# Kernel tuning notes

Hardware: AMD Instinct MI355X
Metric: run time of the kernel (lower is better)

The kernel has to match this reference:

```python
import jax, jax.numpy as jnp
import numpy as np

N_NODES = 50000
N_EDGES = 800000
D = 128
N_LAYERS = 4


def _sage_conv(x, edge_index, Wl, bl, Wr):
    # PyG SAGEConv (mean aggr): out = lin_l(mean_{j in N(i)} x_j) + lin_r(x_i)
    src, dst = edge_index[0], edge_index[1]
    msgs = x[src]                                            # [E, D] gather
    summed = jax.ops.segment_sum(msgs, dst, num_segments=N_NODES)   # [N, D]
    cnt = jax.ops.segment_sum(jnp.ones((msgs.shape[0],), x.dtype), dst,
                              num_segments=N_NODES)
    mean = summed / jnp.maximum(cnt, 1.0)[:, None]           # [N, D]
    return mean @ Wl.T + bl + x @ Wr.T


def setup_inputs() -> dict:
    key = jax.random.key(0)
    ks = jax.random.split(key, 2 + 3 * N_LAYERS)
    x = jax.random.normal(ks[0], (N_NODES, D), dtype=jnp.float32)
    edge_index = jax.random.randint(ks[1], (2, N_EDGES), 0, N_NODES, dtype=jnp.int64)
    inp = {"x": x, "edge_index": edge_index}
    s = 1.0 / np.sqrt(D)
    for i in range(N_LAYERS):
        inp[f"Wl{i}"] = jax.random.uniform(ks[2 + 3 * i], (D, D), jnp.float32, -s, s)
        inp[f"bl{i}"] = jax.random.uniform(ks[3 + 3 * i], (D,), jnp.float32, -s, s)
        inp[f"Wr{i}"] = jax.random.uniform(ks[4 + 3 * i], (D, D), jnp.float32, -s, s)
    return inp


def reference(x, edge_index, Wl0, bl0, Wr0, Wl1, bl1, Wr1, Wl2, bl2, Wr2, Wl3, bl3, Wr3):
    # ReLU only after the first conv, per the original forward.
    h = jax.nn.relu(_sage_conv(x, edge_index, Wl0, bl0, Wr0))
    h = _sage_conv(h, edge_index, Wl1, bl1, Wr1)
    h = _sage_conv(h, edge_index, Wl2, bl2, Wr2)
    h = _sage_conv(h, edge_index, Wl3, bl3, Wr3)
    return h
```

## Files before the change

### kernel.cpp

```cpp
#include <hip/hip_runtime.h>
#include <stdint.h>

#define NN 50000
#define NE 800000
#define CAST_B 6250
#define CVTW_B 512
#define EPB 8192
#define HIST_B 98
#define NBK 196

typedef short short8 __attribute__((ext_vector_type(8)));
typedef float f32x4 __attribute__((ext_vector_type(4)));
typedef unsigned int uint;
typedef unsigned short ushort;

__device__ __forceinline__ uint rne_bf16(float f) {
    uint x = __float_as_uint(f);
    return (x + 0x7FFFu + ((x >> 16) & 1u)) >> 16;
}
__device__ __forceinline__ float bf_lo(uint d) { return __uint_as_float(d << 16); }
__device__ __forceinline__ float bf_hi(uint d) { return __uint_as_float(d & 0xFFFF0000u); }

__device__ __forceinline__ int ei_is64(const int* __restrict__ ei) {
    return (ei[1] | ei[3] | ei[5] | ei[7]) == 0;
}

struct Ptrs8 { const float* p[8]; };

__global__ __launch_bounds__(256) void k_prep(
    const float* __restrict__ x, ushort* __restrict__ xbf, Ptrs8 ps,
    ushort* __restrict__ wbf, const int* __restrict__ ei,
    uint* __restrict__ ebuf, int* __restrict__ hcnt) {
    __shared__ int hs[NBK];
    int b = blockIdx.x;
    if (b < CAST_B) {
        int i = b * 256 + threadIdx.x;
        float4 v = ((const float4*)x)[i];
        uint2 o;
        o.x = rne_bf16(v.x) | (rne_bf16(v.y) << 16);
        o.y = rne_bf16(v.z) | (rne_bf16(v.w) << 16);
        ((uint2*)xbf)[i] = o;
    } else if (b < CAST_B + CVTW_B) {
        int idx = (b - CAST_B) * 256 + threadIdx.x;
        int m = idx >> 14;
        int o14 = idx & 16383;
        int k0i = (o14 >> 12) & 3;
        int t = (o14 >> 9) & 7;
        int lane6 = (o14 >> 3) & 63;
        int e = o14 & 7;
        int r = t * 16 + (lane6 & 15);
        int c = k0i * 32 + (lane6 >> 4) * 8 + e;
        wbf[idx] = (ushort)rne_bf16(ps.p[m][r * 128 + c]);
    } else {
        int hb = b - CAST_B - CVTW_B;
        int t = threadIdx.x;
        for (int i = t; i < NBK; i += 256) hs[i] = 0;
        __syncthreads();
        int base = hb * EPB;
        int is64 = ei_is64(ei);
        for (int i = 0; i < EPB; i += 256) {
            int e = base + i + t;
            if (e < NE) {
                int sv = is64 ? ei[2 * e] : ei[e];
                int dv = is64 ? ei[2 * NE + 2 * e] : ei[NE + e];
                ebuf[e] = ((uint)dv << 16) | (uint)sv;
                atomicAdd(&hs[dv >> 8], 1);
            }
        }
        __syncthreads();
        for (int i = t; i < NBK; i += 256) hcnt[hb * NBK + i] = hs[i];
    }
}

__global__ __launch_bounds__(256) void k_scan1(const int* __restrict__ hcnt,
                                               int* __restrict__ hoff,
                                               int* __restrict__ bb,
                                               int* __restrict__ row_ptr) {
    __shared__ int s[256];
    int t = threadIdx.x;
    int tot = 0;
    if (t < NBK)
        for (int b = 0; b < HIST_B; b++) tot += hcnt[b * NBK + t];
    s[t] = tot;
    __syncthreads();
    for (int off = 1; off < 256; off <<= 1) {
        int v = s[t];
        int a = (t >= off) ? s[t - off] : 0;
        __syncthreads();
        s[t] = v + a;
        __syncthreads();
    }
    if (t < NBK) {
        int base = (t == 0) ? 0 : s[t - 1];
        bb[t] = base;
        int run = base;
        for (int b = 0; b < HIST_B; b++) {
            hoff[b * NBK + t] = run;
            run += hcnt[b * NBK + t];
        }
    }
    if (t == 0) { bb[NBK] = NE; row_ptr[NN] = NE; }
}

__global__ __launch_bounds__(256) void k_scatter1(const uint* __restrict__ ebuf,
                                                  const int* __restrict__ hoff,
                                                  uint* __restrict__ ebuf2) {
    __shared__ int pos[NBK];
    int hb = blockIdx.x, t = threadIdx.x;
    for (int i = t; i < NBK; i += 256) pos[i] = hoff[hb * NBK + i];
    __syncthreads();
    int base = hb * EPB;
    for (int i = 0; i < EPB; i += 256) {
        int e = base + i + t;
        if (e < NE) {
            uint pk = ebuf[e];
            int idx = atomicAdd(&pos[pk >> 24], 1);
            ebuf2[idx] = pk;
        }
    }
}

__global__ __launch_bounds__(1024) void k_sort2(const uint* __restrict__ ebuf2,
                                                const int* __restrict__ bb,
                                                int* __restrict__ row_ptr,
                                                ushort* __restrict__ col) {
    __shared__ int hist[256];
    __shared__ int pos[256];
    int k = blockIdx.x, t = threadIdx.x;
    int beg = bb[k], end = bb[k + 1];
    if (t < 256) hist[t] = 0;
    __syncthreads();
    for (int j = beg + t; j < end; j += 1024)
        atomicAdd(&hist[(ebuf2[j] >> 16) & 255], 1);
    __syncthreads();
    for (int off = 1; off < 256; off <<= 1) {
        int v = 0;
        if (t < 256) { v = hist[t]; if (t >= off) v += hist[t - off]; }
        __syncthreads();
        if (t < 256) hist[t] = v;
        __syncthreads();
    }
    if (t < 256) {
        int ex = (t == 0) ? 0 : hist[t - 1];
        pos[t] = beg + ex;
        int node = k * 256 + t;
        if (node < NN) row_ptr[node] = beg + ex;
    }
    __syncthreads();
    for (int j = beg + t; j < end; j += 1024) {
        uint pk = ebuf2[j];
        int idx = atomicAdd(&pos[(pk >> 16) & 255], 1);
        col[idx] = (ushort)(pk & 0xFFFFu);
    }
}

__global__ __launch_bounds__(256) void k_agg3(const ushort* __restrict__ h,
                                              const int* __restrict__ row_ptr,
                                              const ushort* __restrict__ col,
                                              ushort* __restrict__ mean) {
    int node = blockIdx.x * 4 + (threadIdx.x >> 6);
    if (node >= NN) return;
    int lane = threadIdx.x & 63;
    int beg = row_ptr[node], end = row_ptr[node + 1];
    const uint* hp = (const uint*)h;
    float a0 = 0.f, a1 = 0.f;
    for (int b = beg; b < end; b += 64) {
        int n = min(64, end - b);
        int c = (int)col[b + min(lane, n - 1)];
        for (int j0 = 0; j0 < n; j0 += 8) {
#pragma unroll
            for (int j = 0; j < 8; j++) {
                int jj = j0 + j;
                int s = __shfl(c, min(jj, n - 1));
                uint v = hp[s * 64 + lane];
                float m = (jj < n) ? 1.f : 0.f;
                a0 = fmaf(m, bf_lo(v), a0);
                a1 = fmaf(m, bf_hi(v), a1);
            }
        }
    }
    float r = 1.0f / (float)max(end - beg, 1);
    ((uint*)mean)[node * 64 + lane] = rne_bf16(a0 * r) | (rne_bf16(a1 * r) << 16);
}

__global__ __launch_bounds__(256) void k_gemm_mfma(
    const ushort* __restrict__ Am, const ushort* __restrict__ Ah,
    const ushort* __restrict__ Wlb, const ushort* __restrict__ Wrb,
    const float* __restrict__ bias, float* __restrict__ outf,
    ushort* __restrict__ outb, int relu) {
    const int lane = threadIdx.x & 63;
    const int wave = threadIdx.x >> 6;
    const int l15 = lane & 15;
    const int quad = lane >> 4;
    const int m0 = blockIdx.x * 128 + wave * 32;

    f32x4 acc[2][8];
#pragma unroll
    for (int s = 0; s < 2; s++)
#pragma unroll
        for (int t = 0; t < 8; t++) acc[s][t] = (f32x4){0.f, 0.f, 0.f, 0.f};

    int ar0 = min(m0 + l15, NN - 1);
    int ar1 = min(m0 + 16 + l15, NN - 1);
    const ushort* A0m = Am + (size_t)ar0 * 128 + quad * 8;
    const ushort* A1m = Am + (size_t)ar1 * 128 + quad * 8;
    const ushort* A0h = Ah + (size_t)ar0 * 128 + quad * 8;
    const ushort* A1h = Ah + (size_t)ar1 * 128 + quad * 8;

#pragma unroll
    for (int half = 0; half < 2; half++) {
        const ushort* W = half ? Wrb : Wlb;
        const ushort* A0 = half ? A0h : A0m;
        const ushort* A1 = half ? A1h : A1m;
#pragma unroll
        for (int k0 = 0; k0 < 128; k0 += 32) {
            short8 a0 = *(const short8*)(A0 + k0);
            short8 a1 = *(const short8*)(A1 + k0);
            const ushort* Wk = W + ((k0 >> 5) * 8) * 512 + lane * 8;
#pragma unroll
            for (int t = 0; t < 8; t++) {
                short8 b = *(const short8*)(Wk + t * 512);
                acc[0][t] = __builtin_amdgcn_mfma_f32_16x16x32_bf16(a0, b, acc[0][t], 0, 0, 0);
                acc[1][t] = __builtin_amdgcn_mfma_f32_16x16x32_bf16(a1, b, acc[1][t], 0, 0, 0);
            }
        }
    }

    float bb[8];
#pragma unroll
    for (int t = 0; t < 8; t++) bb[t] = bias[t * 16 + l15];

#pragma unroll
    for (int s = 0; s < 2; s++) {
#pragma unroll
        for (int r = 0; r < 4; r++) {
            int row = m0 + s * 16 + quad * 4 + r;
            if (row < NN) {
#pragma unroll
                for (int t = 0; t < 8; t++) {
                    float v = acc[s][t][r] + bb[t];
                    if (relu) v = fmaxf(v, 0.f);
                    if (outb) outb[(size_t)row * 128 + t * 16 + l15] = (ushort)rne_bf16(v);
                    else outf[(size_t)row * 128 + t * 16 + l15] = v;
                }
            }
        }
    }
}

extern "C" void kernel_launch(void* const* d_in, const int* in_sizes, int n_in,
                              void* d_out, int out_size, void* d_ws, size_t ws_size,
                              hipStream_t stream) {
    const float* x = (const float*)d_in[0];
    const int* ei = (const int*)d_in[1];
    const float* Wl[4] = {(const float*)d_in[2], (const float*)d_in[5],
                          (const float*)d_in[8], (const float*)d_in[11]};
    const float* bl[4] = {(const float*)d_in[3], (const float*)d_in[6],
                          (const float*)d_in[9], (const float*)d_in[12]};
    const float* Wr[4] = {(const float*)d_in[4], (const float*)d_in[7],
                          (const float*)d_in[10], (const float*)d_in[13]};
    float* out = (float*)d_out;

    char* p = (char*)d_ws;
    auto take = [&](size_t bytes) -> char* {
        char* r = p;
        p += (bytes + 255) & ~(size_t)255;
        return r;
    };
    uint* ebuf = (uint*)take((size_t)NE * 4);
    uint* ebuf2 = (uint*)take((size_t)NE * 4);
    int* hcnt = (int*)take((size_t)HIST_B * NBK * 4);
    int* hoff = (int*)take((size_t)HIST_B * NBK * 4);
    int* bb = (int*)take((NBK + 1) * 4);
    int* row_ptr = (int*)take((NN + 1) * 4);
    ushort* col = (ushort*)take((size_t)NE * 2 + 256);
    ushort* xbf = (ushort*)take((size_t)NN * 128 * 2);
    ushort* h1 = (ushort*)take((size_t)NN * 128 * 2);
    ushort* h2 = (ushort*)take((size_t)NN * 128 * 2);
    ushort* meanbf = (ushort*)take((size_t)NN * 128 * 2);
    ushort* wbf = (ushort*)take(8 * 16384 * 2);

    Ptrs8 ps;
    ps.p[0] = Wl[0]; ps.p[1] = Wr[0]; ps.p[2] = Wl[1]; ps.p[3] = Wr[1];
    ps.p[4] = Wl[2]; ps.p[5] = Wr[2]; ps.p[6] = Wl[3]; ps.p[7] = Wr[3];

    k_prep<<<CAST_B + CVTW_B + HIST_B, 256, 0, stream>>>(x, xbf, ps, wbf, ei,
                                                         ebuf, hcnt);
    k_scan1<<<1, 256, 0, stream>>>(hcnt, hoff, bb, row_ptr);
    k_scatter1<<<HIST_B, 256, 0, stream>>>(ebuf, hoff, ebuf2);
    k_sort2<<<NBK, 1024, 0, stream>>>(ebuf2, bb, row_ptr, col);

    const ushort* h = xbf;
    ushort* houts[4] = {h1, h2, h1, nullptr};
    for (int l = 0; l < 4; l++) {
        k_agg3<<<(NN + 3) / 4, 256, 0, stream>>>(h, row_ptr, col, meanbf);
        k_gemm_mfma<<<(NN + 127) / 128, 256, 0, stream>>>(
            meanbf, h, wbf + (size_t)(2 * l) * 16384,
            wbf + (size_t)(2 * l + 1) * 16384, bl[l], out, houts[l],
            l == 0 ? 1 : 0);
        h = houts[l];
    }
}
```

Baseline: 353.6 us.

## Slab-partition CSR by source range and aggregate 8 nodes per wave

The CSR sort now also buckets each node's edges into 7 source-index slabs (src>>13), giving a per-node 8-entry row pointer. The aggregation kernel has each wave handle 8 nodes and walk the slabs in order with a block barrier between slabs, so concurrent gathers hit a narrower range of h rows and issue 8 independent loads per step. The aim is better L2 locality and more memory-level parallelism in the gather-heavy aggregation. In exchange the sort does a larger 2048-bin scan, the row-pointer array is 8x bigger, and waves whose 8 nodes have uneven slab degrees spend masked iterations.

```diff
diff --git a/kernel.cpp b/kernel.cpp
--- a/kernel.cpp
+++ b/kernel.cpp
@@ -8,6 +8,8 @@
 #define EPB 8192
 #define HIST_B 98
 #define NBK 196
+#define NSLAB 7
+#define AGG_B 1564
 
 typedef short short8 __attribute__((ext_vector_type(8)));
 typedef float f32x4 __attribute__((ext_vector_type(4)));
@@ -74,8 +76,7 @@
 
 __global__ __launch_bounds__(256) void k_scan1(const int* __restrict__ hcnt,
                                                int* __restrict__ hoff,
-                                               int* __restrict__ bb,
-                                               int* __restrict__ row_ptr) {
+                                               int* __restrict__ bb) {
     __shared__ int s[256];
     int t = threadIdx.x;
     int tot = 0;
@@ -99,7 +100,7 @@
             run += hcnt[b * NBK + t];
         }
     }
-    if (t == 0) { bb[NBK] = NE; row_ptr[NN] = NE; }
+    if (t == 0) bb[NBK] = NE;
 }
 
 __global__ __launch_bounds__(256) void k_scatter1(const uint* __restrict__ ebuf,
@@ -122,65 +123,123 @@
 
 __global__ __launch_bounds__(1024) void k_sort2(const uint* __restrict__ ebuf2,
                                                 const int* __restrict__ bb,
-                                                int* __restrict__ row_ptr,
+                                                int* __restrict__ row_ptr2,
                                                 ushort* __restrict__ col) {
-    __shared__ int hist[256];
-    __shared__ int pos[256];
+    __shared__ int hist[2048];
+    __shared__ int pos[2048];
     int k = blockIdx.x, t = threadIdx.x;
     int beg = bb[k], end = bb[k + 1];
-    if (t < 256) hist[t] = 0;
-    __syncthreads();
-    for (int j = beg + t; j < end; j += 1024)
-        atomicAdd(&hist[(ebuf2[j] >> 16) & 255], 1);
-    __syncthreads();
-    for (int off = 1; off < 256; off <<= 1) {
-        int v = 0;
-        if (t < 256) { v = hist[t]; if (t >= off) v += hist[t - off]; }
-        __syncthreads();
-        if (t < 256) hist[t] = v;
-        __syncthreads();
-    }
-    if (t < 256) {
-        int ex = (t == 0) ? 0 : hist[t - 1];
-        pos[t] = beg + ex;
-        int node = k * 256 + t;
-        if (node < NN) row_ptr[node] = beg + ex;
-    }
+    hist[t] = 0;
+    hist[t + 1024] = 0;
     __syncthreads();
     for (int j = beg + t; j < end; j += 1024) {
         uint pk = ebuf2[j];
-        int idx = atomicAdd(&pos[(pk >> 16) & 255], 1);
+        int f = (((pk >> 16) & 255) << 3) | ((pk & 0xFFFFu) >> 13);
+        atomicAdd(&hist[f], 1);
+    }
+    __syncthreads();
+    for (int off = 1; off < 1024; off <<= 1) {
+        int v0 = hist[t], v1 = hist[1024 + t];
+        int a0 = (t >= off) ? hist[t - off] : 0;
+        int a1 = (t >= off) ? hist[1024 + t - off] : 0;
+        __syncthreads();
+        hist[t] = v0 + a0;
+        hist[1024 + t] = v1 + a1;
+        __syncthreads();
+    }
+    int tot0 = hist[1023];
+    __syncthreads();
+    hist[1024 + t] += tot0;
+    __syncthreads();
+    for (int b = t; b < 2048; b += 1024) {
+        int ex = (b == 0) ? 0 : hist[b - 1];
+        pos[b] = beg + ex;
+        int node = k * 256 + (b >> 3);
+        if (node < NN) row_ptr2[node * 8 + (b & 7)] = beg + ex;
+    }
+    if (k == 0 && t == 0) row_ptr2[NN * 8] = NE;
+    __syncthreads();
+    for (int j = beg + t; j < end; j += 1024) {
+        uint pk = ebuf2[j];
+        int f = (((pk >> 16) & 255) << 3) | ((pk & 0xFFFFu) >> 13);
+        int idx = atomicAdd(&pos[f], 1);
         col[idx] = (ushort)(pk & 0xFFFFu);
     }
 }
 
-__global__ __launch_bounds__(256) void k_agg3(const ushort* __restrict__ h,
-                                              const int* __restrict__ row_ptr,
-                                              const ushort* __restrict__ col,
-                                              ushort* __restrict__ mean) {
-    int node = blockIdx.x * 4 + (threadIdx.x >> 6);
-    if (node >= NN) return;
-    int lane = threadIdx.x & 63;
-    int beg = row_ptr[node], end = row_ptr[node + 1];
+__global__ __launch_bounds__(256, 6) void k_agg5(
+    const ushort* __restrict__ h, const int* __restrict__ rp2,
+    const ushort* __restrict__ col, ushort* __restrict__ mean) {
+    const int wid = threadIdx.x >> 6;
+    const int lane = threadIdx.x & 63;
+    const int n0 = blockIdx.x * 32 + wid * 8;
     const uint* hp = (const uint*)h;
-    float a0 = 0.f, a1 = 0.f;
-    for (int b = beg; b < end; b += 64) {
-        int n = min(64, end - b);
-        int c = (int)col[b + min(lane, n - 1)];
-        for (int j0 = 0; j0 < n; j0 += 8) {
-#pragma unroll
-            for (int j = 0; j < 8; j++) {
-                int jj = j0 + j;
-                int s = __shfl(c, min(jj, n - 1));
-                uint v = hp[s * 64 + lane];
-                float m = (jj < n) ? 1.f : 0.f;
-                a0 = fmaf(m, bf_lo(v), a0);
-                a1 = fmaf(m, bf_hi(v), a1);
-            }
-        }
-    }
-    float r = 1.0f / (float)max(end - beg, 1);
-    ((uint*)mean)[node * 64 + lane] = rne_bf16(a0 * r) | (rne_bf16(a1 * r) << 16);
+    float a0[8], a1[8];
+    int dg[8];
+#pragma unroll
+    for (int ni = 0; ni < 8; ni++) { a0[ni] = 0.f; a1[ni] = 0.f; dg[ni] = 0; }
+
+    for (int g = 0; g < NSLAB; g++) {
+        int len[8], cc[8];
+#pragma unroll
+        for (int ni = 0; ni < 8; ni++) {
+            int node = n0 + ni;
+            int beg = 0, end = 0;
+            if (node < NN) {
+                int2 be = *(const int2*)&rp2[node * 8 + g];
+                beg = be.x; end = be.y;
+            }
+            int L = end - beg;
+            len[ni] = L;
+            dg[ni] += L;
+            cc[ni] = (int)col[beg + min(lane, max(L - 1, 0))];
+        }
+        int ml = 0;
+#pragma unroll
+        for (int ni = 0; ni < 8; ni++) ml = max(ml, len[ni]);
+        ml = min(ml, 64);
+        for (int j = 0; j < ml; j++) {
+            uint v[8];
+#pragma unroll
+            for (int ni = 0; ni < 8; ni++) {
+                int s = __shfl(cc[ni], min(j, max(len[ni] - 1, 0)));
+                v[ni] = hp[(size_t)s * 64 + lane];
+            }
+#pragma unroll
+            for (int ni = 0; ni < 8; ni++) {
+                float m = (j < len[ni]) ? 1.f : 0.f;
+                a0[ni] = fmaf(m, bf_lo(v[ni]), a0[ni]);
+                a1[ni] = fmaf(m, bf_hi(v[ni]), a1[ni]);
+            }
+        }
+#pragma unroll
+        for (int ni = 0; ni < 8; ni++) {
+            if (__builtin_expect(len[ni] > 64, 0)) {
+                int node = n0 + ni;
+                int2 be = *(const int2*)&rp2[node * 8 + g];
+                for (int b = be.x + 64; b < be.y; b += 64) {
+                    int n = min(64, be.y - b);
+                    int c = (int)col[b + min(lane, n - 1)];
+                    for (int j = 0; j < n; j++) {
+                        int s = __shfl(c, j);
+                        uint v = hp[(size_t)s * 64 + lane];
+                        a0[ni] += bf_lo(v);
+                        a1[ni] += bf_hi(v);
+                    }
+                }
+            }
+        }
+        __syncthreads();
+    }
+#pragma unroll
+    for (int ni = 0; ni < 8; ni++) {
+        int node = n0 + ni;
+        if (node < NN) {
+            float r = 1.0f / (float)max(dg[ni], 1);
+            ((uint*)mean)[(size_t)node * 64 + lane] =
+                rne_bf16(a0[ni] * r) | (rne_bf16(a1[ni] * r) << 16);
+        }
+    }
 }
 
 __global__ __launch_bounds__(256) void k_gemm_mfma(
@@ -272,7 +331,7 @@
     int* hcnt = (int*)take((size_t)HIST_B * NBK * 4);
     int* hoff = (int*)take((size_t)HIST_B * NBK * 4);
     int* bb = (int*)take((NBK + 1) * 4);
-    int* row_ptr = (int*)take((NN + 1) * 4);
+    int* row_ptr2 = (int*)take(((size_t)NN * 8 + 8) * 4);
     ushort* col = (ushort*)take((size_t)NE * 2 + 256);
     ushort* xbf = (ushort*)take((size_t)NN * 128 * 2);
     ushort* h1 = (ushort*)take((size_t)NN * 128 * 2);
@@ -286,14 +345,14 @@
 
     k_prep<<<CAST_B + CVTW_B + HIST_B, 256, 0, stream>>>(x, xbf, ps, wbf, ei,
                                                          ebuf, hcnt);
-    k_scan1<<<1, 256, 0, stream>>>(hcnt, hoff, bb, row_ptr);
+    k_scan1<<<1, 256, 0, stream>>>(hcnt, hoff, bb);
     k_scatter1<<<HIST_B, 256, 0, stream>>>(ebuf, hoff, ebuf2);
-    k_sort2<<<NBK, 1024, 0, stream>>>(ebuf2, bb, row_ptr, col);
+    k_sort2<<<NBK, 1024, 0, stream>>>(ebuf2, bb, row_ptr2, col);
 
     const ushort* h = xbf;
     ushort* houts[4] = {h1, h2, h1, nullptr};
     for (int l = 0; l < 4; l++) {
-        k_agg3<<<(NN + 3) / 4, 256, 0, stream>>>(h, row_ptr, col, meanbf);
+        k_agg5<<<AGG_B, 256, 0, stream>>>(h, row_ptr2, col, meanbf);
         k_gemm_mfma<<<(NN + 127) / 128, 256, 0, stream>>>(
             meanbf, h, wbf + (size_t)(2 * l) * 16384,
             wbf + (size_t)(2 * l + 1) * 16384, bl[l], out, houts[l],
```

Result: slower. 556.1 us (+57.3%).
